# Optimization experiments

Hardware: AMD Instinct MI355X
Metric: run time of the kernel (lower is better)

The kernel has to match this reference:

```python
import jax, jax.numpy as jnp
import numpy as np

# AccumulateKnn with distances == 1.0 everywhere and n_moments=0:
# weight w = exp(-distance) = exp(-1); output = concat(mean_k(w*f), max_k(w*f))
_W = float(np.exp(-1.0))


def _accumulate_knn(features, idx):
    # features: [N, F], idx: [N, K] -> [N, 2F]
    g = features[idx]                      # [N, K, F] neighbour gather
    mean = jnp.mean(g, axis=1) * _W        # [N, F]
    mx = jnp.max(g, axis=1) * _W           # [N, F]
    return jnp.concatenate([mean, mx], axis=-1)


def setup_inputs() -> dict:
    key = jax.random.key(0)
    k1, k2, k3, k4 = jax.random.split(key, 4)
    N, K, F = 200000, 32, 64
    x = jax.random.normal(k1, (N, F), dtype=jnp.float32)
    neighbour_indices = jax.random.randint(k2, (N, K), 0, N, dtype=jnp.int64)
    W0 = jax.random.normal(k3, (F, 64), dtype=jnp.float32) * (1.0 / np.sqrt(F))
    b0 = jnp.zeros((64,), dtype=jnp.float32)
    W1 = jax.random.normal(k4, (128, 64), dtype=jnp.float32) * (1.0 / np.sqrt(128))
    b1 = jnp.zeros((64,), dtype=jnp.float32)
    return {"x": x, "neighbour_indices": neighbour_indices,
            "W0": W0, "b0": b0, "W1": W1, "b1": b1}


def reference(x, neighbour_indices, W0, b0, W1, b1):
    allfeat = []
    feats = x
    for (W, b) in ((W0, b0), (W1, b1)):
        f = jax.nn.relu(feats @ W + b)            # dense + ReLU, [N, F_i]
        coll = _accumulate_knn(f, neighbour_indices)  # [N, 2*F_i]
        # subtract tiled self features: tile(f,[1,2]) == concat([f,f],-1)
        out = coll - jnp.concatenate([f, f], axis=-1)
        allfeat.append(out)
        feats = out
    return jnp.concatenate(allfeat + [x], axis=-1)  # [N, 128+128+64]
```

## Files before the change

### kernel.cpp

```cpp
#include <hip/hip_runtime.h>
#include <hip/hip_bf16.h>

typedef __hip_bfloat16 bf16;

__device__ __forceinline__ float us2f(unsigned short u) {
  union { unsigned int ui; float f; } cv; cv.ui = ((unsigned int)u) << 16; return cv.f;
}
__device__ __forceinline__ unsigned short f2us(float f) {
  union { float f; unsigned int u; } cv; cv.f = f;
  unsigned int u = cv.u;
  return (unsigned short)((u + 0x7fffu + ((u >> 16) & 1u)) >> 16);
}

#define WEXP 0.36787944117144233f

template<int KDIM>
__global__ __launch_bounds__(256) void dense_relu_kernel(
    const float* __restrict__ in, int in_stride,
    const float* __restrict__ W, const float* __restrict__ b,
    bf16* __restrict__ fout, float* __restrict__ xcopy, int n)
{
  __shared__ float Ws[KDIM][68];
  __shared__ float Xs[32][KDIM + 1];
  const int tx = threadIdx.x;
  const int row0 = blockIdx.x * 32;

  for (int t = tx; t < KDIM * 16; t += 256) {
    float4 w4 = ((const float4*)W)[t];
    int k = t >> 4, c4 = (t & 15) * 4;
    Ws[k][c4 + 0] = w4.x; Ws[k][c4 + 1] = w4.y; Ws[k][c4 + 2] = w4.z; Ws[k][c4 + 3] = w4.w;
  }

  constexpr int CH = KDIM / 4;
  for (int t = tx; t < 32 * CH; t += 256) {
    int rr = t / CH, kc = t - rr * CH;
    int row = row0 + rr;
    float4 f4 = make_float4(0.f, 0.f, 0.f, 0.f);
    if (row < n)
      f4 = *(const float4*)(in + (size_t)row * in_stride + kc * 4);
    Xs[rr][kc * 4 + 0] = f4.x; Xs[rr][kc * 4 + 1] = f4.y;
    Xs[rr][kc * 4 + 2] = f4.z; Xs[rr][kc * 4 + 3] = f4.w;
    if (xcopy != nullptr && row < n)
      *(float4*)(xcopy + (size_t)row * 320 + kc * 4) = f4;
  }
  __syncthreads();

  const int c = tx & 15;
  const int r = tx >> 4;
  float acc0[4] = {0.f, 0.f, 0.f, 0.f};
  float acc1[4] = {0.f, 0.f, 0.f, 0.f};
#pragma unroll 8
  for (int k = 0; k < KDIM; ++k) {
    const float4 w4 = *(const float4*)&Ws[k][c * 4];
    const float x0 = Xs[2 * r][k];
    const float x1 = Xs[2 * r + 1][k];
    acc0[0] += x0 * w4.x; acc0[1] += x0 * w4.y; acc0[2] += x0 * w4.z; acc0[3] += x0 * w4.w;
    acc1[0] += x1 * w4.x; acc1[1] += x1 * w4.y; acc1[2] += x1 * w4.z; acc1[3] += x1 * w4.w;
  }

  const float4 bb = *(const float4*)&b[c * 4];

  int row = row0 + 2 * r;
  if (row < n) {
    ushort4 o;
    o.x = f2us(fmaxf(acc0[0] + bb.x, 0.f));
    o.y = f2us(fmaxf(acc0[1] + bb.y, 0.f));
    o.z = f2us(fmaxf(acc0[2] + bb.z, 0.f));
    o.w = f2us(fmaxf(acc0[3] + bb.w, 0.f));
    *(ushort4*)((unsigned short*)fout + (size_t)row * 64 + c * 4) = o;
  }
  row = row0 + 2 * r + 1;
  if (row < n) {
    ushort4 o;
    o.x = f2us(fmaxf(acc1[0] + bb.x, 0.f));
    o.y = f2us(fmaxf(acc1[1] + bb.y, 0.f));
    o.z = f2us(fmaxf(acc1[2] + bb.z, 0.f));
    o.w = f2us(fmaxf(acc1[3] + bb.w, 0.f));
    *(ushort4*)((unsigned short*)fout + (size_t)row * 64 + c * 4) = o;
  }
}

__global__ __launch_bounds__(256) void accum_kernel(
    const bf16* __restrict__ f,
    const int* __restrict__ idx,
    float* __restrict__ out,
    int n)
{
  const int wid = threadIdx.x >> 6;
  const int lane = threadIdx.x & 63;
  const int i = blockIdx.x * 4 + wid;
  if (i >= n) return;

  int iv = 0;
  if (lane < 32) iv = idx[(size_t)i * 32 + lane];

  const float self = us2f(((const unsigned short*)f)[(size_t)i * 64 + lane]);

  float sum = 0.f, mx = -3.4e38f;
#pragma unroll
  for (int k = 0; k < 32; ++k) {
    int nk = __shfl(iv, k);
    float v = us2f(((const unsigned short*)f)[(size_t)nk * 64 + lane]);
    sum += v;
    mx = fmaxf(mx, v);
  }

  const float meanv = sum * (WEXP / 32.0f);
  const float maxv = mx * WEXP;
  float* o = out + (size_t)i * 320 + lane;
  o[0] = meanv - self;
  o[64] = maxv - self;
}

extern "C" void kernel_launch(void* const* d_in, const int* in_sizes, int n_in,
                              void* d_out, int out_size, void* d_ws, size_t ws_size,
                              hipStream_t stream) {
  const float* x  = (const float*)d_in[0];
  const int* idx  = (const int*)d_in[1];
  const float* W0 = (const float*)d_in[2];
  const float* b0 = (const float*)d_in[3];
  const float* W1 = (const float*)d_in[4];
  const float* b1 = (const float*)d_in[5];
  float* out = (float*)d_out;
  const int n = in_sizes[0] / 64;

  bf16* fbuf = (bf16*)d_ws;

  const int dblocks = (n + 31) / 32;
  const int ablocks = (n + 3) / 4;

  dense_relu_kernel<64><<<dblocks, 256, 0, stream>>>(x, 64, W0, b0, fbuf, out + 256, n);
  accum_kernel<<<ablocks, 256, 0, stream>>>(fbuf, idx, out, n);
  dense_relu_kernel<128><<<dblocks, 256, 0, stream>>>(out, 320, W1, b1, fbuf, nullptr, n);
  accum_kernel<<<ablocks, 256, 0, stream>>>(fbuf, idx, out + 128, n);
}
```

Baseline: 599.7 us.

## Vectorize neighbour gather to 16-byte loads with cross-lane reduction

Each wavefront now gathers neighbour rows with 16-byte uint4 loads. Eight lanes cover one 64-feature bf16 row, so eight neighbours are read per load step instead of one 2-byte load per lane per neighbour. Partial sums and maxima over the 8 features each lane holds are combined across lane groups with xor shuffles, and the mean and max outputs are written as float4 stores by two lane groups. This cuts the number of memory instructions per gathered row, at the cost of more registers and shuffle traffic, and only a quarter of lanes take part in the output stores.

```diff
diff --git a/kernel.cpp b/kernel.cpp
--- a/kernel.cpp
+++ b/kernel.cpp
@@ -10,6 +10,12 @@
   union { float f; unsigned int u; } cv; cv.f = f;
   unsigned int u = cv.u;
   return (unsigned short)((u + 0x7fffu + ((u >> 16) & 1u)) >> 16);
+}
+__device__ __forceinline__ float lo2f(unsigned int u) {
+  union { unsigned int ui; float f; } cv; cv.ui = u << 16; return cv.f;
+}
+__device__ __forceinline__ float hi2f(unsigned int u) {
+  union { unsigned int ui; float f; } cv; cv.ui = u & 0xffff0000u; return cv.f;
 }
 
 #define WEXP 0.36787944117144233f
@@ -94,22 +100,66 @@
   int iv = 0;
   if (lane < 32) iv = idx[(size_t)i * 32 + lane];
 
-  const float self = us2f(((const unsigned short*)f)[(size_t)i * 64 + lane]);
+  const int L = lane & 7;
+  const int srcbase = (lane >> 3) << 2;
 
-  float sum = 0.f, mx = -3.4e38f;
+  float s[8], m[8];
 #pragma unroll
-  for (int k = 0; k < 32; ++k) {
-    int nk = __shfl(iv, k);
-    float v = us2f(((const unsigned short*)f)[(size_t)nk * 64 + lane]);
-    sum += v;
-    mx = fmaxf(mx, v);
+  for (int j = 0; j < 8; ++j) { s[j] = 0.f; m[j] = -3.4e38f; }
+
+  const char* fb = (const char*)f;
+#pragma unroll
+  for (int t = 0; t < 4; ++t) {
+    const int nk = __shfl(iv, srcbase + t);
+    const unsigned off = (((unsigned)nk) << 7) + ((unsigned)L << 4);
+    const uint4 d = *(const uint4*)(fb + off);
+    float v;
+    v = lo2f(d.x); s[0] += v; m[0] = fmaxf(m[0], v);
+    v = hi2f(d.x); s[1] += v; m[1] = fmaxf(m[1], v);
+    v = lo2f(d.y); s[2] += v; m[2] = fmaxf(m[2], v);
+    v = hi2f(d.y); s[3] += v; m[3] = fmaxf(m[3], v);
+    v = lo2f(d.z); s[4] += v; m[4] = fmaxf(m[4], v);
+    v = hi2f(d.z); s[5] += v; m[5] = fmaxf(m[5], v);
+    v = lo2f(d.w); s[6] += v; m[6] = fmaxf(m[6], v);
+    v = hi2f(d.w); s[7] += v; m[7] = fmaxf(m[7], v);
   }
 
-  const float meanv = sum * (WEXP / 32.0f);
-  const float maxv = mx * WEXP;
-  float* o = out + (size_t)i * 320 + lane;
-  o[0] = meanv - self;
-  o[64] = maxv - self;
+#pragma unroll
+  for (int off = 8; off <= 32; off <<= 1) {
+#pragma unroll
+    for (int j = 0; j < 8; ++j) {
+      s[j] += __shfl_xor(s[j], off);
+      m[j] = fmaxf(m[j], __shfl_xor(m[j], off));
+    }
+  }
+
+  const uint4 sd = *(const uint4*)(fb + (((unsigned)i) << 7) + ((unsigned)L << 4));
+  float self[8];
+  self[0] = lo2f(sd.x); self[1] = hi2f(sd.x);
+  self[2] = lo2f(sd.y); self[3] = hi2f(sd.y);
+  self[4] = lo2f(sd.z); self[5] = hi2f(sd.z);
+  self[6] = lo2f(sd.w); self[7] = hi2f(sd.w);
+
+  const float cmean = WEXP / 32.0f;
+  const int o = lane >> 3;
+  float* orow = out + (size_t)i * 320;
+  if (o == 0) {
+    float4 a, bq;
+    a.x = s[0] * cmean - self[0]; a.y = s[1] * cmean - self[1];
+    a.z = s[2] * cmean - self[2]; a.w = s[3] * cmean - self[3];
+    bq.x = s[4] * cmean - self[4]; bq.y = s[5] * cmean - self[5];
+    bq.z = s[6] * cmean - self[6]; bq.w = s[7] * cmean - self[7];
+    *(float4*)(orow + 8 * L) = a;
+    *(float4*)(orow + 8 * L + 4) = bq;
+  } else if (o == 1) {
+    float4 a, bq;
+    a.x = m[0] * WEXP - self[0]; a.y = m[1] * WEXP - self[1];
+    a.z = m[2] * WEXP - self[2]; a.w = m[3] * WEXP - self[3];
+    bq.x = m[4] * WEXP - self[4]; bq.y = m[5] * WEXP - self[5];
+    bq.z = m[6] * WEXP - self[6]; bq.w = m[7] * WEXP - self[7];
+    *(float4*)(orow + 64 + 8 * L) = a;
+    *(float4*)(orow + 64 + 8 * L + 4) = bq;
+  }
 }
 
 extern "C" void kernel_launch(void* const* d_in, const int* in_sizes, int n_in,
```

Result: no change. 603.6 us (+0.6%).
